# Optimization experiments

Measured on AMD Instinct MI355X. Metric: run time of the kernel, lower is better.

## Reference

```python
import jax, jax.numpy as jnp
import numpy as np

SIZE = 1024
N_HEAD = 16
HEAD_DIM = SIZE // N_HEAD


def setup_inputs() -> dict:
    key = jax.random.key(0)
    ks = jax.random.split(key, 5)
    s = 1.0 / np.sqrt(SIZE)
    return {
        "x": jax.random.normal(ks[0], (4, 2048, SIZE), dtype=jnp.float32),
        "w_qkv": jax.random.uniform(ks[1], (SIZE, 3 * SIZE), dtype=jnp.float32, minval=-s, maxval=s),
        "b_qkv": jax.random.uniform(ks[2], (3 * SIZE,), dtype=jnp.float32, minval=-s, maxval=s),
        "w_fc": jax.random.uniform(ks[3], (SIZE, SIZE), dtype=jnp.float32, minval=-s, maxval=s),
        "b_fc": jax.random.uniform(ks[4], (SIZE,), dtype=jnp.float32, minval=-s, maxval=s),
    }


def reference(x, w_qkv, b_qkv, w_fc, b_fc):
    B, S, D = x.shape
    qkv = x @ w_qkv + b_qkv                      # [B, S, 3D]
    qkv = qkv.reshape(B, S, 3, N_HEAD, HEAD_DIM)
    qkv = jnp.transpose(qkv, (2, 0, 3, 1, 4))    # [3, B, H, S, hd]
    q, k, v = qkv[0], qkv[1], qkv[2]
    scale = 1.0 / np.sqrt(HEAD_DIM).astype(np.float32)
    scores = jnp.einsum('bhqd,bhkd->bhqk', q, k) * scale
    attn = jax.nn.softmax(scores, axis=-1)
    out = jnp.einsum('bhqk,bhkd->bhqd', attn, v)  # [B, H, S, hd]
    out = jnp.transpose(out, (0, 2, 1, 3)).reshape(B, S, D)
    return out @ w_fc + b_fc
```

## Files before the change

kernel.cpp:

```cpp
#include <hip/hip_runtime.h>

#define DEV __device__ __forceinline__

typedef float  f32x4   __attribute__((ext_vector_type(4)));
typedef float  f32x16  __attribute__((ext_vector_type(16)));
typedef short  short8  __attribute__((ext_vector_type(8)));
typedef __bf16 bf16x8  __attribute__((ext_vector_type(8)));
typedef unsigned u32x2 __attribute__((ext_vector_type(2)));
typedef unsigned u32x4 __attribute__((ext_vector_type(4)));

DEV f32x4 mfma_bf16(short8 a, short8 b, f32x4 c) {
    return __builtin_amdgcn_mfma_f32_16x16x32_bf16(
        __builtin_bit_cast(bf16x8, a), __builtin_bit_cast(bf16x8, b), c, 0, 0, 0);
}

DEV f32x16 mfma32(short8 a, short8 b, f32x16 c) {
    return __builtin_amdgcn_mfma_f32_32x32x16_bf16(
        __builtin_bit_cast(bf16x8, a), __builtin_bit_cast(bf16x8, b), c, 0, 0, 0);
}

DEV void gload_lds16(const void* g, void* l) {
    __builtin_amdgcn_global_load_lds(
        (const __attribute__((address_space(1))) unsigned int*)g,
        (__attribute__((address_space(3))) unsigned int*)l, 16, 0, 0);
}

DEV short f2bf(float f) { return __builtin_bit_cast(short, (__bf16)f); }

DEV unsigned pack_bf2(float lo, float hi) {
    unsigned short a = __builtin_bit_cast(unsigned short, (__bf16)lo);
    unsigned short b = __builtin_bit_cast(unsigned short, (__bf16)hi);
    return ((unsigned)b << 16) | (unsigned)a;
}

DEV u32x2 pl32swap(unsigned a, unsigned b) {
    return __builtin_amdgcn_permlane32_swap(a, b, false, false);
}

__global__ void cast_x(const float* __restrict__ in, unsigned short* __restrict__ out, int n) {
    int i = (blockIdx.x * 256 + threadIdx.x) * 8;
    if (i >= n) return;
    f32x4 a = *(const f32x4*)(in + i);
    f32x4 b = *(const f32x4*)(in + i + 4);
    short8 o;
    o[0] = f2bf(a[0]); o[1] = f2bf(a[1]); o[2] = f2bf(a[2]); o[3] = f2bf(a[3]);
    o[4] = f2bf(b[0]); o[5] = f2bf(b[1]); o[6] = f2bf(b[2]); o[7] = f2bf(b[3]);
    *(short8*)(out + i) = o;
}

__global__ void transpose_cast(const float* __restrict__ in, unsigned short* __restrict__ out,
                               int R, int C) {
    __shared__ float tile[64][65];
    int c0 = blockIdx.x * 64, r0 = blockIdx.y * 64;
    int tx = threadIdx.x & 63, ty = threadIdx.x >> 6;
#pragma unroll
    for (int i = 0; i < 16; i++) {
        int r = i * 4 + ty;
        tile[r][tx] = in[(size_t)(r0 + r) * C + c0 + tx];
    }
    __syncthreads();
#pragma unroll
    for (int i = 0; i < 16; i++) {
        int cc = i * 4 + ty;
        out[(size_t)(c0 + cc) * R + r0 + tx] = (unsigned short)f2bf(tile[tx][cc]);
    }
}

__global__ void transpose_v(const unsigned short* __restrict__ Vb,
                            unsigned short* __restrict__ Vt) {
    __shared__ __align__(16) unsigned short tile[64][72];
    const int t = threadIdx.x;
    const int s0 = blockIdx.x * 64;
    const size_t slab = (size_t)blockIdx.y * 2048 * 64;
#pragma unroll
    for (int i = 0; i < 2; i++) {
        int c = i * 256 + t;
        int s = c >> 3, ch = c & 7;
        short8 v = *(const short8*)(Vb + slab + (size_t)(s0 + s) * 64 + ch * 8);
        *(short8*)(&tile[s][ch * 8]) = v;
    }
    __syncthreads();
#pragma unroll
    for (int i = 0; i < 2; i++) {
        int c = i * 256 + t;
        int d = c & 63, sc = c >> 6;
        short8 o;
#pragma unroll
        for (int e = 0; e < 8; e++) o[e] = tile[sc * 8 + e][d];
        *(short8*)(Vt + slab + (size_t)d * 2048 + s0 + sc * 8) = o;
    }
}

template <int MODE>
__global__ __launch_bounds__(256, 2) void gemm_bt(
    const unsigned short* __restrict__ A, const unsigned short* __restrict__ Bt,
    const float* __restrict__ bias, float* __restrict__ out_f32,
    unsigned short* __restrict__ q_out, unsigned short* __restrict__ k_out,
    unsigned short* __restrict__ v_out, int K) {
    __shared__ __align__(16) char smem[32768];
    char* lA = smem;
    char* lB = smem + 16384;
    const int t = threadIdx.x;
    const int lane = t & 63, w = t >> 6;
    const int wr = w >> 1, wc = w & 1;
    const int rowBase = blockIdx.y * 128, colBase = blockIdx.x * 128;

    f32x4 acc[4][4] = {};

    for (int k0 = 0; k0 < K; k0 += 64) {
#pragma unroll
        for (int i = 0; i < 4; i++) {
            int c = i * 256 + t;
            int r = c >> 3, j = c & 7;
            int jj = j ^ (r & 7);
            gload_lds16(A  + (size_t)(rowBase + r) * K + k0 + jj * 8, lA + c * 16);
            gload_lds16(Bt + (size_t)(colBase + r) * K + k0 + jj * 8, lB + c * 16);
        }
        __syncthreads();
#pragma unroll
        for (int ks = 0; ks < 2; ks++) {
            const int colb = (ks * 4 + (lane >> 4)) * 16;
            short8 af[4], bfr[4];
#pragma unroll
            for (int m2 = 0; m2 < 4; m2++) {
                int r = wr * 64 + m2 * 16 + (lane & 15);
                af[m2] = *(const short8*)(lA + r * 128 + (colb ^ ((r & 7) << 4)));
            }
#pragma unroll
            for (int n2 = 0; n2 < 4; n2++) {
                int r = wc * 64 + n2 * 16 + (lane & 15);
                bfr[n2] = *(const short8*)(lB + r * 128 + (colb ^ ((r & 7) << 4)));
            }
#pragma unroll
            for (int m2 = 0; m2 < 4; m2++)
#pragma unroll
                for (int n2 = 0; n2 < 4; n2++)
                    acc[m2][n2] = mfma_bf16(af[m2], bfr[n2], acc[m2][n2]);
        }
        __syncthreads();
    }

#pragma unroll
    for (int n2 = 0; n2 < 4; n2++) {
        int gc = colBase + wc * 64 + n2 * 16 + (lane & 15);
        float bv = bias[gc];
#pragma unroll
        for (int m2 = 0; m2 < 4; m2++) {
            int grb = rowBase + wr * 64 + m2 * 16 + ((lane >> 4) << 2);
#pragma unroll
            for (int r2 = 0; r2 < 4; r2++) {
                int gr = grb + r2;
                float v = acc[m2][n2][r2] + bv;
                if (MODE == 0) {
                    int which = gc >> 10, rem = gc & 1023;
                    int h = rem >> 6, d = rem & 63;
                    int b = gr >> 11, s = gr & 2047;
                    size_t idx = ((size_t)((b * 16 + h) * 2048 + s)) * 64 + d;
                    unsigned short* dst = which == 0 ? q_out : (which == 1 ? k_out : v_out);
                    if (which == 0) v *= 0.18033688011112042f;
                    dst[idx] = (unsigned short)f2bf(v);
                } else {
                    out_f32[(size_t)gr * 1024 + gc] = v;
                }
            }
        }
    }
}

__global__ __launch_bounds__(256, 4) void fattn(
    const unsigned short* __restrict__ Qb, const unsigned short* __restrict__ Kb,
    const unsigned short* __restrict__ Vt, unsigned short* __restrict__ O) {
    __shared__ __align__(16) char smem[32768];
    const int t = threadIdx.x, lane = t & 63, w = t >> 6;
    const int h = lane >> 5, l5 = lane & 31;
    const int bh = blockIdx.y;
    const int q0 = blockIdx.x * 128 + w * 32;
    const size_t slab = (size_t)bh * 2048 * 64;

    short8 qf[4];
#pragma unroll
    for (int s = 0; s < 4; s++)
        qf[s] = *(const short8*)(Qb + slab + (size_t)(q0 + l5) * 64 + s * 16 + h * 8);

#define STAGE_KV(kv0, buf)                                                          \
    do {                                                                            \
        char* dK_ = smem + (buf) * 8192;                                            \
        char* dV_ = smem + 16384 + (buf) * 8192;                                    \
        _Pragma("unroll")                                                           \
        for (int i_ = 0; i_ < 2; i_++) {                                            \
            int c_ = i_ * 256 + t, r_ = c_ >> 3, j_ = c_ & 7, jj_ = j_ ^ (r_ & 7);  \
            gload_lds16(Kb + slab + (size_t)((kv0) + r_) * 64 + jj_ * 8,            \
                        dK_ + c_ * 16);                                             \
            gload_lds16(Vt + slab + (size_t)r_ * 2048 + (kv0) + jj_ * 8,            \
                        dV_ + c_ * 16);                                             \
        }                                                                           \
    } while (0)

    STAGE_KV(0, 0);

    float lsum = 0.f;
    f32x16 accO0 = {}, accO1 = {};

    int cur = 0;
    for (int kt = 0; kt < 32; kt++) {
        __syncthreads();
        if (kt < 31) STAGE_KV((kt + 1) * 64, cur ^ 1);
        char* lKc = smem + cur * 8192;
        char* lVc = smem + 16384 + cur * 8192;

        f32x16 st0 = {}, st1 = {};
#pragma unroll
        for (int s = 0; s < 4; s++) {
            const int cb = s * 32 + h * 16;
            short8 k0 = *(const short8*)(lKc + l5 * 128 + (cb ^ ((l5 & 7) << 4)));
            short8 k1 = *(const short8*)(lKc + (32 + l5) * 128 + (cb ^ ((l5 & 7) << 4)));
            st0 = mfma32(k0, qf[s], st0);
            st1 = mfma32(k1, qf[s], st1);
        }

#pragma unroll
        for (int kv2 = 0; kv2 < 2; kv2++) {
            const f32x16 stc = kv2 ? st1 : st0;
            unsigned pk[8];
#pragma unroll
            for (int i = 0; i < 8; i++) {
                float p0 = __builtin_amdgcn_exp2f(stc[2 * i]);
                float p1 = __builtin_amdgcn_exp2f(stc[2 * i + 1]);
                lsum += p0 + p1;
                pk[i] = pack_bf2(p0, p1);
            }
            u32x2 s02 = pl32swap(pk[0], pk[2]);
            u32x2 s13 = pl32swap(pk[1], pk[3]);
            u32x2 s46 = pl32swap(pk[4], pk[6]);
            u32x2 s57 = pl32swap(pk[5], pk[7]);
            u32x4 af0 = {s02[0], s13[0], s02[1], s13[1]};
            u32x4 af1 = {s46[0], s57[0], s46[1], s57[1]};
#pragma unroll
            for (int s = 0; s < 2; s++) {
                short8 ap = __builtin_bit_cast(short8, s == 0 ? af0 : af1);
                const int cb = kv2 * 64 + s * 32 + h * 16;
                short8 v0 = *(const short8*)(lVc + l5 * 128 + (cb ^ ((l5 & 7) << 4)));
                short8 v1 = *(const short8*)(lVc + (32 + l5) * 128 + (cb ^ ((l5 & 7) << 4)));
                accO0 = mfma32(ap, v0, accO0);
                accO1 = mfma32(ap, v1, accO1);
            }
        }
        cur ^= 1;
    }
#undef STAGE_KV

    lsum += __shfl_xor(lsum, 32);
    float inv = 1.f / lsum;

    const int b = bh >> 4, hh = bh & 15;
#pragma unroll
    for (int r = 0; r < 16; r++) {
        int row = (r & 3) + 8 * (r >> 2) + 4 * h;
        float iv = __shfl(inv, row, 64);
        size_t base = ((size_t)(b * 2048 + q0 + row)) * 1024 + hh * 64;
        O[base + l5]      = (unsigned short)f2bf(accO0[r] * iv);
        O[base + 32 + l5] = (unsigned short)f2bf(accO1[r] * iv);
    }
}

extern "C" void kernel_launch(void* const* d_in, const int* in_sizes, int n_in,
                              void* d_out, int out_size, void* d_ws, size_t ws_size,
                              hipStream_t stream) {
    const float* x     = (const float*)d_in[0];
    const float* w_qkv = (const float*)d_in[1];
    const float* b_qkv = (const float*)d_in[2];
    const float* w_fc  = (const float*)d_in[3];
    const float* b_fc  = (const float*)d_in[4];

    char* ws = (char*)d_ws;
    unsigned short* Xb    = (unsigned short*)(ws);
    unsigned short* WqkvT = (unsigned short*)(ws + 16777216);
    unsigned short* WfcT  = (unsigned short*)(ws + 23068672);
    unsigned short* Qb    = (unsigned short*)(ws + 25165824);
    unsigned short* Kb    = (unsigned short*)(ws + 41943040);
    unsigned short* Vb    = (unsigned short*)(ws + 58720256);
    unsigned short* Ao    = (unsigned short*)(ws + 75497472);
    unsigned short* Vt    = Xb;

    cast_x<<<dim3(8388608 / (256 * 8)), 256, 0, stream>>>(x, Xb, 8388608);
    transpose_cast<<<dim3(3072 / 64, 1024 / 64), 256, 0, stream>>>(w_qkv, WqkvT, 1024, 3072);
    transpose_cast<<<dim3(1024 / 64, 1024 / 64), 256, 0, stream>>>(w_fc, WfcT, 1024, 1024);

    gemm_bt<0><<<dim3(3072 / 128, 8192 / 128), 256, 0, stream>>>(
        Xb, WqkvT, b_qkv, nullptr, Qb, Kb, Vb, 1024);

    transpose_v<<<dim3(32, 64), 256, 0, stream>>>(Vb, Vt);

    fattn<<<dim3(16, 64), 256, 0, stream>>>(Qb, Kb, Vt, Ao);

    gemm_bt<1><<<dim3(1024 / 128, 8192 / 128), 256, 0, stream>>>(
        Ao, WfcT, b_fc, (float*)d_out, nullptr, nullptr, nullptr, 1024);
}
```

Before: 276.8 us.

## Fuse V transpose into QKV GEMM epilogue, add XCD swizzle and MFMA priority hints

The QKV GEMM epilogue now writes V directly in transposed [d][s] layout with 4-wide packed stores, which removes the separate transpose_v kernel and its extra round trip through memory. Both GEMMs and the attention kernel remap block IDs with an XCD-aware swizzle so neighbouring tiles share L2. MFMA sections are bracketed with s_setprio. The softmax pack uses v_cvt_pk_bf16_f32 inline asm, and the row-sum accumulates into four partial registers to break the add dependency chain. The strided V stores and the swizzle may change cache behaviour in ways that are hard to foresee.

```diff
diff --git a/kernel.cpp b/kernel.cpp
--- a/kernel.cpp
+++ b/kernel.cpp
@@ -4,6 +4,7 @@
 
 typedef float  f32x4   __attribute__((ext_vector_type(4)));
 typedef float  f32x16  __attribute__((ext_vector_type(16)));
+typedef short  s16x4   __attribute__((ext_vector_type(4)));
 typedef short  short8  __attribute__((ext_vector_type(8)));
 typedef __bf16 bf16x8  __attribute__((ext_vector_type(8)));
 typedef unsigned u32x2 __attribute__((ext_vector_type(2)));
@@ -27,14 +28,19 @@
 
 DEV short f2bf(float f) { return __builtin_bit_cast(short, (__bf16)f); }
 
-DEV unsigned pack_bf2(float lo, float hi) {
-    unsigned short a = __builtin_bit_cast(unsigned short, (__bf16)lo);
-    unsigned short b = __builtin_bit_cast(unsigned short, (__bf16)hi);
-    return ((unsigned)b << 16) | (unsigned)a;
+DEV unsigned cvt_pk_bf16(float lo, float hi) {
+    unsigned r;
+    asm("v_cvt_pk_bf16_f32 %0, %1, %2" : "=v"(r) : "v"(lo), "v"(hi));
+    return r;
 }
 
 DEV u32x2 pl32swap(unsigned a, unsigned b) {
     return __builtin_amdgcn_permlane32_swap(a, b, false, false);
+}
+
+DEV int xcd_swz(int fid, int nwg) {
+    int cpx = nwg >> 3;
+    return (fid & 7) * cpx + (fid >> 3);
 }
 
 __global__ void cast_x(const float* __restrict__ in, unsigned short* __restrict__ out, int n) {
@@ -63,31 +69,6 @@
     for (int i = 0; i < 16; i++) {
         int cc = i * 4 + ty;
         out[(size_t)(c0 + cc) * R + r0 + tx] = (unsigned short)f2bf(tile[tx][cc]);
-    }
-}
-
-__global__ void transpose_v(const unsigned short* __restrict__ Vb,
-                            unsigned short* __restrict__ Vt) {
-    __shared__ __align__(16) unsigned short tile[64][72];
-    const int t = threadIdx.x;
-    const int s0 = blockIdx.x * 64;
-    const size_t slab = (size_t)blockIdx.y * 2048 * 64;
-#pragma unroll
-    for (int i = 0; i < 2; i++) {
-        int c = i * 256 + t;
-        int s = c >> 3, ch = c & 7;
-        short8 v = *(const short8*)(Vb + slab + (size_t)(s0 + s) * 64 + ch * 8);
-        *(short8*)(&tile[s][ch * 8]) = v;
-    }
-    __syncthreads();
-#pragma unroll
-    for (int i = 0; i < 2; i++) {
-        int c = i * 256 + t;
-        int d = c & 63, sc = c >> 6;
-        short8 o;
-#pragma unroll
-        for (int e = 0; e < 8; e++) o[e] = tile[sc * 8 + e][d];
-        *(short8*)(Vt + slab + (size_t)d * 2048 + s0 + sc * 8) = o;
     }
 }
 
@@ -103,7 +84,9 @@
     const int t = threadIdx.x;
     const int lane = t & 63, w = t >> 6;
     const int wr = w >> 1, wc = w & 1;
-    const int rowBase = blockIdx.y * 128, colBase = blockIdx.x * 128;
+    const int nbx = gridDim.x;
+    const int sw = xcd_swz(blockIdx.y * nbx + blockIdx.x, nbx * gridDim.y);
+    const int rowBase = (sw / nbx) * 128, colBase = (sw % nbx) * 128;
 
     f32x4 acc[4][4] = {};
 
@@ -131,37 +114,70 @@
                 int r = wc * 64 + n2 * 16 + (lane & 15);
                 bfr[n2] = *(const short8*)(lB + r * 128 + (colb ^ ((r & 7) << 4)));
             }
+            __builtin_amdgcn_s_setprio(1);
 #pragma unroll
             for (int m2 = 0; m2 < 4; m2++)
 #pragma unroll
                 for (int n2 = 0; n2 < 4; n2++)
                     acc[m2][n2] = mfma_bf16(af[m2], bfr[n2], acc[m2][n2]);
+            __builtin_amdgcn_s_setprio(0);
         }
         __syncthreads();
     }
 
-#pragma unroll
-    for (int n2 = 0; n2 < 4; n2++) {
-        int gc = colBase + wc * 64 + n2 * 16 + (lane & 15);
-        float bv = bias[gc];
-#pragma unroll
-        for (int m2 = 0; m2 < 4; m2++) {
-            int grb = rowBase + wr * 64 + m2 * 16 + ((lane >> 4) << 2);
-#pragma unroll
-            for (int r2 = 0; r2 < 4; r2++) {
-                int gr = grb + r2;
-                float v = acc[m2][n2][r2] + bv;
-                if (MODE == 0) {
-                    int which = gc >> 10, rem = gc & 1023;
-                    int h = rem >> 6, d = rem & 63;
-                    int b = gr >> 11, s = gr & 2047;
-                    size_t idx = ((size_t)((b * 16 + h) * 2048 + s)) * 64 + d;
-                    unsigned short* dst = which == 0 ? q_out : (which == 1 ? k_out : v_out);
-                    if (which == 0) v *= 0.18033688011112042f;
-                    dst[idx] = (unsigned short)f2bf(v);
-                } else {
-                    out_f32[(size_t)gr * 1024 + gc] = v;
+    if (MODE == 0) {
+        const int which = colBase >> 10;
+        if (which == 2) {
+#pragma unroll
+            for (int n2 = 0; n2 < 4; n2++) {
+                int gc = colBase + wc * 64 + n2 * 16 + (lane & 15);
+                int rem = gc & 1023;
+                int h = rem >> 6, d = rem & 63;
+                float bv = bias[gc];
+#pragma unroll
+                for (int m2 = 0; m2 < 4; m2++) {
+                    int grb = rowBase + wr * 64 + m2 * 16 + ((lane >> 4) << 2);
+                    int b = grb >> 11, s = grb & 2047;
+                    s16x4 o;
+#pragma unroll
+                    for (int r2 = 0; r2 < 4; r2++) o[r2] = f2bf(acc[m2][n2][r2] + bv);
+                    *(s16x4*)(v_out + ((size_t)((b * 16 + h) * 64 + d)) * 2048 + s) = o;
                 }
+            }
+        } else {
+            const float qs = which == 0 ? 0.18033688011112042f : 1.0f;
+            unsigned short* dst = which == 0 ? q_out : k_out;
+#pragma unroll
+            for (int n2 = 0; n2 < 4; n2++) {
+                int gc = colBase + wc * 64 + n2 * 16 + (lane & 15);
+                int rem = gc & 1023;
+                int h = rem >> 6, d = rem & 63;
+                float bv = bias[gc];
+#pragma unroll
+                for (int m2 = 0; m2 < 4; m2++) {
+                    int grb = rowBase + wr * 64 + m2 * 16 + ((lane >> 4) << 2);
+#pragma unroll
+                    for (int r2 = 0; r2 < 4; r2++) {
+                        int gr = grb + r2;
+                        int b = gr >> 11, s = gr & 2047;
+                        float v = (acc[m2][n2][r2] + bv) * qs;
+                        dst[((size_t)((b * 16 + h) * 2048 + s)) * 64 + d] =
+                            (unsigned short)f2bf(v);
+                    }
+                }
+            }
+        }
+    } else {
+#pragma unroll
+        for (int n2 = 0; n2 < 4; n2++) {
+            int gc = colBase + wc * 64 + n2 * 16 + (lane & 15);
+            float bv = bias[gc];
+#pragma unroll
+            for (int m2 = 0; m2 < 4; m2++) {
+                int grb = rowBase + wr * 64 + m2 * 16 + ((lane >> 4) << 2);
+#pragma unroll
+                for (int r2 = 0; r2 < 4; r2++)
+                    out_f32[(size_t)(grb + r2) * 1024 + gc] = acc[m2][n2][r2] + bv;
             }
         }
     }
@@ -173,8 +189,9 @@
     __shared__ __align__(16) char smem[32768];
     const int t = threadIdx.x, lane = t & 63, w = t >> 6;
     const int h = lane >> 5, l5 = lane & 31;
-    const int bh = blockIdx.y;
-    const int q0 = blockIdx.x * 128 + w * 32;
+    const int sw = xcd_swz(blockIdx.x, 1024);
+    const int bh = sw >> 4;
+    const int q0 = (sw & 15) * 128 + w * 32;
     const size_t slab = (size_t)bh * 2048 * 64;
 
     short8 qf[4];
@@ -198,7 +215,7 @@
 
     STAGE_KV(0, 0);
 
-    float lsum = 0.f;
+    f32x4 lsum4 = {};
     f32x16 accO0 = {}, accO1 = {};
 
     int cur = 0;
@@ -209,6 +226,7 @@
         char* lVc = smem + 16384 + cur * 8192;
 
         f32x16 st0 = {}, st1 = {};
+        __builtin_amdgcn_s_setprio(1);
 #pragma unroll
         for (int s = 0; s < 4; s++) {
             const int cb = s * 32 + h * 16;
@@ -217,6 +235,7 @@
             st0 = mfma32(k0, qf[s], st0);
             st1 = mfma32(k1, qf[s], st1);
         }
+        __builtin_amdgcn_s_setprio(0);
 
 #pragma unroll
         for (int kv2 = 0; kv2 < 2; kv2++) {
@@ -226,8 +245,8 @@
             for (int i = 0; i < 8; i++) {
                 float p0 = __builtin_amdgcn_exp2f(stc[2 * i]);
                 float p1 = __builtin_amdgcn_exp2f(stc[2 * i + 1]);
-                lsum += p0 + p1;
-                pk[i] = pack_bf2(p0, p1);
+                lsum4[i & 3] += p0 + p1;
+                pk[i] = cvt_pk_bf16(p0, p1);
             }
             u32x2 s02 = pl32swap(pk[0], pk[2]);
             u32x2 s13 = pl32swap(pk[1], pk[3]);
@@ -235,6 +254,7 @@
             u32x2 s57 = pl32swap(pk[5], pk[7]);
             u32x4 af0 = {s02[0], s13[0], s02[1], s13[1]};
             u32x4 af1 = {s46[0], s57[0], s46[1], s57[1]};
+            __builtin_amdgcn_s_setprio(1);
 #pragma unroll
             for (int s = 0; s < 2; s++) {
                 short8 ap = __builtin_bit_cast(short8, s == 0 ? af0 : af1);
@@ -244,11 +264,13 @@
                 accO0 = mfma32(ap, v0, accO0);
                 accO1 = mfma32(ap, v1, accO1);
             }
+            __builtin_amdgcn_s_setprio(0);
         }
         cur ^= 1;
     }
 #undef STAGE_KV
 
+    float lsum = lsum4[0] + lsum4[1] + lsum4[2] + lsum4[3];
     lsum += __shfl_xor(lsum, 32);
     float inv = 1.f / lsum;
 
@@ -278,20 +300,17 @@
     unsigned short* WfcT  = (unsigned short*)(ws + 23068672);
     unsigned short* Qb    = (unsigned short*)(ws + 25165824);
     unsigned short* Kb    = (unsigned short*)(ws + 41943040);
-    unsigned short* Vb    = (unsigned short*)(ws + 58720256);
+    unsigned short* Vt    = (unsigned short*)(ws + 58720256);
     unsigned short* Ao    = (unsigned short*)(ws + 75497472);
-    unsigned short* Vt    = Xb;
 
     cast_x<<<dim3(8388608 / (256 * 8)), 256, 0, stream>>>(x, Xb, 8388608);
     transpose_cast<<<dim3(3072 / 64, 1024 / 64), 256, 0, stream>>>(w_qkv, WqkvT, 1024, 3072);
     transpose_cast<<<dim3(1024 / 64, 1024 / 64), 256, 0, stream>>>(w_fc, WfcT, 1024, 1024);
 
     gemm_bt<0><<<dim3(3072 / 128, 8192 / 128), 256, 0, stream>>>(
-        Xb, WqkvT, b_qkv, nullptr, Qb, Kb, Vb, 1024);
-
-    transpose_v<<<dim3(32, 64), 256, 0, stream>>>(Vb, Vt);
-
-    fattn<<<dim3(16, 64), 256, 0, stream>>>(Qb, Kb, Vt, Ao);
+        Xb, WqkvT, b_qkv, nullptr, Qb, Kb, Vt, 1024);
+
+    fattn<<<dim3(1024), 256, 0, stream>>>(Qb, Kb, Vt, Ao);
 
     gemm_bt<1><<<dim3(1024 / 128, 8192 / 128), 256, 0, stream>>>(
         Ao, WfcT, b_fc, (float*)d_out, nullptr, nullptr, nullptr, 1024);
```

New measurement: 257.8 us. -6.9%, faster.
